# Performance work log

Measured on AMD Instinct MI355X. Metric: run time of the kernel, lower is better.

The kernel has to match this reference:

```python
import jax, jax.numpy as jnp
import numpy as np

D_MODEL = 2048
N_HEADS = 16
KV_HEADS = 4
HEAD_DIM = D_MODEL // N_HEADS            # 128
GROUP = N_HEADS // KV_HEADS              # 4
KV_WIDTH = KV_HEADS * HEAD_DIM           # 512
B, T = 2, 2048


def setup_inputs() -> dict:
    key = jax.random.key(0)
    ks = jax.random.split(key, 5)
    s = 0.02
    x = jax.random.normal(ks[0], (B, T, D_MODEL), dtype=jnp.float32)
    attn_mask = jnp.tril(jnp.ones((T, T), dtype=bool))  # causal
    qkv_w = jax.random.normal(ks[1], (D_MODEL, D_MODEL + 2 * KV_WIDTH), dtype=jnp.float32) * s
    qkv_b = jax.random.normal(ks[2], (D_MODEL + 2 * KV_WIDTH,), dtype=jnp.float32) * s
    proj_w = jax.random.normal(ks[3], (D_MODEL, D_MODEL), dtype=jnp.float32) * s
    proj_b = jax.random.normal(ks[4], (D_MODEL,), dtype=jnp.float32) * s
    return {"x": x, "attn_mask": attn_mask, "qkv_w": qkv_w, "qkv_b": qkv_b,
            "proj_w": proj_w, "proj_b": proj_b}


def reference(x, attn_mask, qkv_w, qkv_b, proj_w, proj_b):
    b, t, c = x.shape
    qkv = x @ qkv_w + qkv_b                               # [b,t,3072]
    q = qkv[..., :D_MODEL]
    k = qkv[..., D_MODEL:D_MODEL + KV_WIDTH]
    v = qkv[..., D_MODEL + KV_WIDTH:]
    # q: [b, kv_heads, group, t, d]; k,v: [b, kv_heads, t, d]
    q = q.reshape(b, t, KV_HEADS, GROUP, HEAD_DIM).transpose(0, 2, 3, 1, 4)
    k = k.reshape(b, t, KV_HEADS, HEAD_DIM).transpose(0, 2, 1, 3)
    v = v.reshape(b, t, KV_HEADS, HEAD_DIM).transpose(0, 2, 1, 3)
    scale = 1.0 / jnp.sqrt(jnp.asarray(HEAD_DIM, dtype=x.dtype))
    att = jnp.einsum('bkgtd,bksd->bkgts', q, k) * scale   # [b,kv,g,t,t]
    att = jnp.where(attn_mask, att, jnp.asarray(-jnp.inf, dtype=att.dtype))
    att = jax.nn.softmax(att, axis=-1)
    out = jnp.einsum('bkgts,bksd->bkgtd', att, v)         # [b,kv,g,t,d]
    out = out.transpose(0, 3, 1, 2, 4).reshape(b, t, c)
    return out @ proj_w + proj_b
```

## Files before the change

### kernel.cpp

```cpp
#include <hip/hip_runtime.h>
#include <cstdint>
#include <cstddef>

#define D_MODEL 2048
#define T_SEQ   2048
#define BATCH   2
#define N_HEADS 16
#define KV_HEADS 4
#define HEAD_DIM 128
#define QKV_N   3072
#define ROWS    (BATCH * T_SEQ)

typedef float  floatx4 __attribute__((ext_vector_type(4)));
typedef short  shortx8 __attribute__((ext_vector_type(8)));
typedef __bf16 bf16x8  __attribute__((ext_vector_type(8)));

typedef const void __attribute__((address_space(1))) gvoid_t;
typedef void __attribute__((address_space(3)))       svoid_t;

__device__ __forceinline__ floatx4 mfma16(shortx8 a, shortx8 b, floatx4 c) {
  return __builtin_amdgcn_mfma_f32_16x16x32_bf16(
      __builtin_bit_cast(bf16x8, a), __builtin_bit_cast(bf16x8, b), c, 0, 0, 0);
}

__device__ __forceinline__ unsigned short f2bf(float f) {
  union { float f; unsigned int u; } v; v.f = f;
  unsigned int u = v.u;
  u += 0x7fffu + ((u >> 16) & 1u);
  return (unsigned short)(u >> 16);
}

__device__ __forceinline__ unsigned short f2bf_hw(float f) {
  return __builtin_bit_cast(unsigned short, (__bf16)f);
}

__global__ void cvt_x(const float* __restrict__ in, unsigned short* __restrict__ out, int n4) {
  int i = blockIdx.x * blockDim.x + threadIdx.x;
  if (i >= n4) return;
  float4 v = ((const float4*)in)[i];
  ushort4 o;
  o.x = f2bf(v.x); o.y = f2bf(v.y); o.z = f2bf(v.z); o.w = f2bf(v.w);
  ((ushort4*)out)[i] = o;
}

__global__ void transpose_cvt(const float* __restrict__ W, unsigned short* __restrict__ Wt,
                              int K, int N) {
  __shared__ float tile[32][33];
  int n0 = blockIdx.x * 32, k0 = blockIdx.y * 32;
  int tx = threadIdx.x, ty = threadIdx.y;
  #pragma unroll
  for (int i = 0; i < 32; i += 8)
    tile[ty + i][tx] = W[(size_t)(k0 + ty + i) * N + n0 + tx];
  __syncthreads();
  #pragma unroll
  for (int i = 0; i < 32; i += 8)
    Wt[(size_t)(n0 + ty + i) * K + k0 + tx] = f2bf(tile[tx][ty + i]);
}

__global__ void build_kt(const unsigned short* __restrict__ qkv, unsigned short* __restrict__ kst) {
  int o = blockIdx.x * blockDim.x + threadIdx.x;
  int t   = o & 2047;
  int d8  = (o >> 11) & 15;
  int kvh = (o >> 15) & 3;
  int b   = o >> 17;
  uint4 v = *(const uint4*)(qkv + (size_t)(b * T_SEQ + t) * QKV_N
                            + D_MODEL + kvh * HEAD_DIM + d8 * 8);
  *(uint4*)(kst + (size_t)o * 8) = v;
}

__global__ void build_vt(const unsigned short* __restrict__ qkv, unsigned short* __restrict__ vst) {
  int o = blockIdx.x * blockDim.x + threadIdx.x;
  int d   = o & 127;
  int t8  = (o >> 7) & 255;
  int kvh = (o >> 15) & 3;
  int b   = o >> 17;
  const unsigned short* src = qkv + (size_t)(b * T_SEQ + t8 * 8) * QKV_N
                              + D_MODEL + 512 + kvh * HEAD_DIM + d;
  union { unsigned short s[8]; uint4 v; } tmp;
  #pragma unroll
  for (int j = 0; j < 8; ++j) tmp.s[j] = src[(size_t)j * QKV_N];
  *(uint4*)(vst + (size_t)o * 8) = tmp.v;
}

__global__ __launch_bounds__(512, 2) void gemm256(
    const unsigned short* __restrict__ A,
    const unsigned short* __restrict__ Bt,
    const float* __restrict__ bias,
    void* __restrict__ Cout,
    int M, int N, int K, int c_bf16)
{
  __shared__ __align__(16) unsigned short lds[65536];
  const int tid  = threadIdx.x;
  const int wave = tid >> 6, lane = tid & 63;
  const int quad = lane >> 4, l16 = lane & 15;
  const int wr = wave >> 2, wc = wave & 3;
  const int bm = blockIdx.y * 256, bn = blockIdx.x * 256;
  const int NT = K >> 6;

  const int r0 = tid >> 3;
  const int cx = (tid & 7) ^ (r0 & 7);
  const size_t K64 = (size_t)64 * K;
  const unsigned short* a_src = A  + (size_t)(bm + r0) * K + cx * 8;
  const unsigned short* b_src = Bt + (size_t)(bn + r0) * K + cx * 8;
  const int wOff = wave * 512;

  #define LDSA_(buf, half) (lds + (((buf) << 1) + (half)) * 8192)
  #define LDSB_(buf, half) (lds + 32768 + (((buf) << 1) + (half)) * 8192)
  #define KOFF(h, t) ((size_t)(h) * 128 * K + (size_t)(t) * 64)
  #define STAGE(srcbase, ldshalf, koff) do {                                          \
    __builtin_amdgcn_global_load_lds((gvoid_t*)((srcbase) + (koff)),                  \
        (svoid_t*)((ldshalf) + wOff), 16, 0, 0);                                      \
    __builtin_amdgcn_global_load_lds((gvoid_t*)((srcbase) + (koff) + K64),            \
        (svoid_t*)((ldshalf) + wOff + 4096), 16, 0, 0);                               \
  } while (0)

  const int rowA = (wr * 64 + l16) * 64;
  const int rowB = (wc * 32 + l16) * 64;
  const int xo0 = ((quad)     ^ (l16 & 7)) * 8;
  const int xo1 = ((4 + quad) ^ (l16 & 7)) * 8;

  floatx4 acc[8][4] = {};
  shortx8 Afr[4][2];
  shortx8 Bfr[4][2];

  STAGE(a_src, LDSA_(0, 0), KOFF(0, 0));
  STAGE(b_src, LDSB_(0, 0), KOFF(0, 0));
  STAGE(b_src, LDSB_(0, 1), KOFF(1, 0));
  STAGE(a_src, LDSA_(0, 1), KOFF(1, 0));
  if (NT > 1) {
    STAGE(a_src, LDSA_(1, 0), KOFF(0, 1));
    STAGE(b_src, LDSB_(1, 0), KOFF(0, 1));
    STAGE(b_src, LDSB_(1, 1), KOFF(1, 1));
  }

  for (int t = 0; t < NT; ++t) {
    const int buf = t & 1;
    unsigned short* sA0 = LDSA_(buf, 0);
    unsigned short* sA1 = LDSA_(buf, 1);
    unsigned short* sB0 = LDSB_(buf, 0);
    unsigned short* sB1 = LDSB_(buf, 1);

    if (t == NT - 1) asm volatile("s_waitcnt vmcnt(0)" ::: "memory");
    else             asm volatile("s_waitcnt vmcnt(6)" ::: "memory");
    __builtin_amdgcn_s_barrier();
    #pragma unroll
    for (int mi = 0; mi < 4; ++mi) {
      Afr[mi][0] = *(const shortx8*)(sA0 + rowA + mi * 1024 + xo0);
      Afr[mi][1] = *(const shortx8*)(sA0 + rowA + mi * 1024 + xo1);
    }
    #pragma unroll
    for (int ni = 0; ni < 2; ++ni) {
      Bfr[ni][0] = *(const shortx8*)(sB0 + rowB + ni * 1024 + xo0);
      Bfr[ni][1] = *(const shortx8*)(sB0 + rowB + ni * 1024 + xo1);
    }
    if (t + 1 < NT) STAGE(a_src, LDSA_(buf ^ 1, 1), KOFF(1, t + 1));
    asm volatile("s_waitcnt lgkmcnt(0)" ::: "memory");
    __builtin_amdgcn_s_setprio(1);
    #pragma unroll
    for (int ks = 0; ks < 2; ++ks)
      #pragma unroll
      for (int mi = 0; mi < 4; ++mi)
        #pragma unroll
        for (int ni = 0; ni < 2; ++ni)
          acc[mi][ni] = mfma16(Afr[mi][ks], Bfr[ni][ks], acc[mi][ni]);
    __builtin_amdgcn_s_setprio(0);
    __builtin_amdgcn_s_barrier();

    #pragma unroll
    for (int ni = 0; ni < 2; ++ni) {
      Bfr[2 + ni][0] = *(const shortx8*)(sB1 + rowB + ni * 1024 + xo0);
      Bfr[2 + ni][1] = *(const shortx8*)(sB1 + rowB + ni * 1024 + xo1);
    }
    if (t + 2 < NT) STAGE(a_src, LDSA_(buf, 0), KOFF(0, t + 2));
    __builtin_amdgcn_s_barrier();
    asm volatile("s_waitcnt lgkmcnt(0)" ::: "memory");
    __builtin_amdgcn_s_setprio(1);
    #pragma unroll
    for (int ks = 0; ks < 2; ++ks)
      #pragma unroll
      for (int mi = 0; mi < 4; ++mi)
        #pragma unroll
        for (int ni = 0; ni < 2; ++ni)
          acc[mi][2 + ni] = mfma16(Afr[mi][ks], Bfr[2 + ni][ks], acc[mi][2 + ni]);
    __builtin_amdgcn_s_setprio(0);
    __builtin_amdgcn_s_barrier();

    #pragma unroll
    for (int mi = 0; mi < 4; ++mi) {
      Afr[mi][0] = *(const shortx8*)(sA1 + rowA + mi * 1024 + xo0);
      Afr[mi][1] = *(const shortx8*)(sA1 + rowA + mi * 1024 + xo1);
    }
    if (t + 2 < NT) STAGE(b_src, LDSB_(buf, 0), KOFF(0, t + 2));
    __builtin_amdgcn_s_barrier();
    asm volatile("s_waitcnt lgkmcnt(0)" ::: "memory");
    __builtin_amdgcn_s_setprio(1);
    #pragma unroll
    for (int ks = 0; ks < 2; ++ks)
      #pragma unroll
      for (int mi = 0; mi < 4; ++mi)
        #pragma unroll
        for (int ni = 0; ni < 2; ++ni)
          acc[4 + mi][2 + ni] = mfma16(Afr[mi][ks], Bfr[2 + ni][ks], acc[4 + mi][2 + ni]);
    __builtin_amdgcn_s_setprio(0);
    __builtin_amdgcn_s_barrier();

    if (t + 2 < NT) STAGE(b_src, LDSB_(buf, 1), KOFF(1, t + 2));
    __builtin_amdgcn_s_barrier();
    __builtin_amdgcn_s_setprio(1);
    #pragma unroll
    for (int ks = 0; ks < 2; ++ks)
      #pragma unroll
      for (int mi = 0; mi < 4; ++mi)
        #pragma unroll
        for (int ni = 0; ni < 2; ++ni)
          acc[4 + mi][ni] = mfma16(Afr[mi][ks], Bfr[ni][ks], acc[4 + mi][ni]);
    __builtin_amdgcn_s_setprio(0);
    __builtin_amdgcn_s_barrier();
  }

  #pragma unroll
  for (int mi = 0; mi < 8; ++mi) {
    const int row = bm + (mi >> 2) * 128 + wr * 64 + (mi & 3) * 16 + quad * 4;
    #pragma unroll
    for (int ni = 0; ni < 4; ++ni) {
      const int col = bn + (ni >> 1) * 128 + wc * 32 + (ni & 1) * 16 + l16;
      const float bv = bias[col];
      #pragma unroll
      for (int r = 0; r < 4; ++r) {
        float v = acc[mi][ni][r] + bv;
        if (c_bf16)
          ((unsigned short*)Cout)[(size_t)(row + r) * N + col] = f2bf_hw(v);
        else
          ((float*)Cout)[(size_t)(row + r) * N + col] = v;
      }
    }
  }
  #undef LDSA_
  #undef LDSB_
  #undef KOFF
  #undef STAGE
}

__global__ __launch_bounds__(256) void attn_kernel(
    const unsigned short* __restrict__ qkv,
    const unsigned short* __restrict__ kst,
    const unsigned short* __restrict__ vst,
    unsigned short* __restrict__ aout)
{
  __shared__ __align__(16) unsigned short sK[2][16 * 64 * 8];
  __shared__ __align__(16) unsigned short sV[2][8 * 128 * 8];
  __shared__ __align__(16) unsigned short sP[4][8 * 16 * 8];

  const int tid  = threadIdx.x;
  const int wave = tid >> 6, lane = tid & 63;
  const int quad = lane >> 4, l16 = lane & 15;
  const int head = blockIdx.y, b = blockIdx.z;
  const int kvh = head >> 2;
  const float cf = 0.08838834764831845f * 1.4426950408889634f;
  const float THR = 25.0f;

  const unsigned short* kbase = kst + (size_t)((b * KV_HEADS + kvh) * 16) * 2048 * 8;
  const unsigned short* vbase = vst + (size_t)((b * KV_HEADS + kvh) * 256) * 128 * 8;
  unsigned short* sPw = sP[wave];

  #define STAGE_KV(dst, kb_) do {                                              \
    _Pragma("unroll")                                                          \
    for (int it_ = 0; it_ < 4; ++it_) {                                        \
      const int c_ = it_ * 4 + wave;                                           \
      __builtin_amdgcn_global_load_lds(                                        \
          (gvoid_t*)(kbase + ((size_t)c_ * 2048 + (kb_)) * 8 + lane * 8),      \
          (svoid_t*)(&sK[dst][c_ * 512]), 16, 0, 0);                           \
    }                                                                          \
    const unsigned short* vt_ = vbase + (size_t)((kb_) >> 3) * 128 * 8;        \
    _Pragma("unroll")                                                          \
    for (int it_ = 0; it_ < 4; ++it_) {                                        \
      const int c_ = it_ * 4 + wave;                                           \
      __builtin_amdgcn_global_load_lds(                                        \
          (gvoid_t*)(vt_ + c_ * 512 + lane * 8),                               \
          (svoid_t*)(&sV[dst][c_ * 512]), 16, 0, 0);                           \
    }                                                                          \
  } while (0)

  #pragma unroll 1
  for (int half = 0; half < 2; ++half) {
    const int qt = half ? blockIdx.x : (31 - blockIdx.x);
    const int q0 = qt * 64;

    shortx8 qf[4];
    {
      const unsigned short* qp = qkv + (size_t)(b * T_SEQ + q0 + wave * 16 + l16) * QKV_N
                                 + head * HEAD_DIM + quad * 8;
      #pragma unroll
      for (int ks = 0; ks < 4; ++ks)
        qf[ks] = *(const shortx8*)(qp + ks * 32);
    }

    float m_i[4], l_i[4];
    #pragma unroll
    for (int r = 0; r < 4; ++r) { m_i[r] = -__builtin_inff(); l_i[r] = 0.f; }
    floatx4 o_acc[8] = {};

    STAGE_KV(0, 0);

    for (int kt = 0; kt <= qt; ++kt) {
      const int cur = kt & 1;
      const unsigned short* sKc = sK[cur];
      const unsigned short* sVc = sV[cur];

      if (kt < qt) {
        STAGE_KV(cur ^ 1, (kt + 1) * 64);
        asm volatile("s_waitcnt vmcnt(8)" ::: "memory");
      } else {
        asm volatile("s_waitcnt vmcnt(0)" ::: "memory");
      }
      __builtin_amdgcn_s_barrier();

      floatx4 s[4] = {};
      __builtin_amdgcn_s_setprio(1);
      #pragma unroll
      for (int ks = 0; ks < 4; ++ks) {
        #pragma unroll
        for (int ct = 0; ct < 4; ++ct) {
          shortx8 kf = *(const shortx8*)&sKc[((ks * 4 + quad) * 64 + ct * 16 + l16) * 8];
          s[ct] = mfma16(qf[ks], kf, s[ct]);
        }
      }
      __builtin_amdgcn_s_setprio(0);

      if (kt == qt) {
        const int qrow = q0 + wave * 16 + quad * 4;
        const int kb = kt * 64;
        #pragma unroll
        for (int ct = 0; ct < 4; ++ct) {
          const int kcol = kb + ct * 16 + l16;
          #pragma unroll
          for (int r = 0; r < 4; ++r)
            if (kcol > qrow + r) s[ct][r] = -__builtin_inff();
        }
      }

      float mx[4];
      #pragma unroll
      for (int r = 0; r < 4; ++r) {
        float m = fmaxf(fmaxf(s[0][r], s[1][r]), fmaxf(s[2][r], s[3][r]));
        m = fmaxf(m, __shfl_xor(m, 1));
        m = fmaxf(m, __shfl_xor(m, 2));
        m = fmaxf(m, __shfl_xor(m, 4));
        m = fmaxf(m, __shfl_xor(m, 8));
        mx[r] = m;
      }

      if (__ballot((mx[0] > m_i[0] + THR) || (mx[1] > m_i[1] + THR) ||
                   (mx[2] > m_i[2] + THR) || (mx[3] > m_i[3] + THR))) {
        float alpha_r[4];
        #pragma unroll
        for (int r = 0; r < 4; ++r) {
          const float newm = fmaxf(m_i[r], mx[r]);
          alpha_r[r] = exp2f((m_i[r] - newm) * cf);
          m_i[r] = newm;
          l_i[r] *= alpha_r[r];
        }
        #pragma unroll
        for (int nt = 0; nt < 8; ++nt)
          #pragma unroll
          for (int r = 0; r < 4; ++r) o_acc[nt][r] *= alpha_r[r];
      }

      #pragma unroll
      for (int r = 0; r < 4; ++r) {
        const float nmc = m_i[r] * cf;
        float p0 = exp2f(fmaf(s[0][r], cf, -nmc));
        float p1 = exp2f(fmaf(s[1][r], cf, -nmc));
        float p2 = exp2f(fmaf(s[2][r], cf, -nmc));
        float p3 = exp2f(fmaf(s[3][r], cf, -nmc));
        s[0][r] = p0; s[1][r] = p1; s[2][r] = p2; s[3][r] = p3;
        l_i[r] += (p0 + p1) + (p2 + p3);
      }

      #pragma unroll
      for (int ct = 0; ct < 4; ++ct)
        #pragma unroll
        for (int r = 0; r < 4; ++r)
          sPw[((ct * 2 + (l16 >> 3)) * 16 + quad * 4 + r) * 8 + (l16 & 7)] = f2bf_hw(s[ct][r]);
      __asm__ __volatile__("s_waitcnt lgkmcnt(0)" ::: "memory");

      __builtin_amdgcn_s_setprio(1);
      #pragma unroll
      for (int ks = 0; ks < 2; ++ks) {
        shortx8 pf = *(const shortx8*)&sPw[((ks * 4 + quad) * 16 + l16) * 8];
        #pragma unroll
        for (int nt = 0; nt < 8; ++nt) {
          shortx8 vf = *(const shortx8*)&sVc[((ks * 4 + quad) * 128 + nt * 16 + l16) * 8];
          o_acc[nt] = mfma16(pf, vf, o_acc[nt]);
        }
      }
      __builtin_amdgcn_s_setprio(0);

      asm volatile("s_waitcnt lgkmcnt(0)" ::: "memory");
      __builtin_amdgcn_s_barrier();
    }

    const int trow = q0 + wave * 16 + quad * 4;
    #pragma unroll
    for (int r = 0; r < 4; ++r) {
      float l = l_i[r];
      l += __shfl_xor(l, 1);
      l += __shfl_xor(l, 2);
      l += __shfl_xor(l, 4);
      l += __shfl_xor(l, 8);
      const float inv = 1.f / l;
      #pragma unroll
      for (int nt = 0; nt < 8; ++nt) {
        aout[(size_t)(b * T_SEQ + trow + r) * D_MODEL + head * HEAD_DIM + nt * 16 + l16] =
            f2bf_hw(o_acc[nt][r] * inv);
      }
    }
  }
  #undef STAGE_KV
}

extern "C" void kernel_launch(void* const* d_in, const int* in_sizes, int n_in,
                              void* d_out, int out_size, void* d_ws, size_t ws_size,
                              hipStream_t stream) {
  const float* x      = (const float*)d_in[0];
  const float* qkv_w  = (const float*)d_in[2];
  const float* qkv_b  = (const float*)d_in[3];
  const float* proj_w = (const float*)d_in[4];
  const float* proj_b = (const float*)d_in[5];
  float* out = (float*)d_out;

  char* ws = (char*)d_ws;
  unsigned short* x_bf    = (unsigned short*)(ws);
  unsigned short* qkvw_t  = (unsigned short*)(ws + (size_t)16777216);
  unsigned short* projw_t = (unsigned short*)(ws + (size_t)29360128);
  unsigned short* qkvbuf  = (unsigned short*)(ws + (size_t)37748736);
  unsigned short* vstaged = (unsigned short*)(ws + (size_t)62914560);
  unsigned short* kstaged = qkvw_t;
  unsigned short* attn_out = x_bf;

  cvt_x<<<(ROWS * D_MODEL / 4 + 255) / 256, 256, 0, stream>>>(x, x_bf, ROWS * D_MODEL / 4);
  transpose_cvt<<<dim3(QKV_N / 32, D_MODEL / 32), dim3(32, 8), 0, stream>>>(qkv_w, qkvw_t, D_MODEL, QKV_N);
  transpose_cvt<<<dim3(D_MODEL / 32, D_MODEL / 32), dim3(32, 8), 0, stream>>>(proj_w, projw_t, D_MODEL, D_MODEL);
  gemm256<<<dim3(QKV_N / 256, ROWS / 256), 512, 0, stream>>>(
      x_bf, qkvw_t, qkv_b, (void*)qkvbuf, ROWS, QKV_N, D_MODEL, 1);
  build_kt<<<1024, 256, 0, stream>>>(qkvbuf, kstaged);
  build_vt<<<1024, 256, 0, stream>>>(qkvbuf, vstaged);
  attn_kernel<<<dim3(16, N_HEADS, BATCH), 256, 0, stream>>>(qkvbuf, kstaged, vstaged, attn_out);
  gemm256<<<dim3(D_MODEL / 256, ROWS / 256), 512, 0, stream>>>(
      attn_out, projw_t, proj_b, (void*)out, ROWS, D_MODEL, D_MODEL, 0);
}
```

Measured before the change: 341.1 us.

## Split attention KV loop across two wave groups with LDS merge

The attention block grows from 4 to 8 waves. Two groups of four waves process even and odd KV tiles for the same 64 query rows, and their online-softmax partial results (m, l, O) are merged through LDS at the end. The goal is more parallelism per block on the sequential causal KV loop, halving its length per wave. In exchange, the double-buffered prefetch pipeline is replaced by a synchronous load-then-wait every iteration. It also adds barriers, a merge step, and higher register pressure under launch_bounds(512,4).

Result: faster. 329.6 us (-3.4%).

```diff
diff --git a/kernel.cpp b/kernel.cpp
--- a/kernel.cpp
+++ b/kernel.cpp
@@ -241,7 +241,7 @@
   #undef STAGE
 }
 
-__global__ __launch_bounds__(256) void attn_kernel(
+__global__ __launch_bounds__(512, 4) void attn_kernel(
     const unsigned short* __restrict__ qkv,
     const unsigned short* __restrict__ kst,
     const unsigned short* __restrict__ vst,
@@ -249,10 +249,11 @@
 {
   __shared__ __align__(16) unsigned short sK[2][16 * 64 * 8];
   __shared__ __align__(16) unsigned short sV[2][8 * 128 * 8];
-  __shared__ __align__(16) unsigned short sP[4][8 * 16 * 8];
+  __shared__ __align__(16) unsigned short sP[8][4 * 16 * 8];
 
   const int tid  = threadIdx.x;
   const int wave = tid >> 6, lane = tid & 63;
+  const int split = wave >> 2, g = wave & 3;
   const int quad = lane >> 4, l16 = lane & 15;
   const int head = blockIdx.y, b = blockIdx.z;
   const int kvh = head >> 2;
@@ -263,21 +264,24 @@
   const unsigned short* vbase = vst + (size_t)((b * KV_HEADS + kvh) * 256) * 128 * 8;
   unsigned short* sPw = sP[wave];
 
-  #define STAGE_KV(dst, kb_) do {                                              \
+  float* mrgO  = (float*)&sK[0][0];
+  float* mrgML = (float*)&sV[0][0];
+
+  #define STAGE_KV(sp, kb_) do {                                               \
     _Pragma("unroll")                                                          \
     for (int it_ = 0; it_ < 4; ++it_) {                                        \
-      const int c_ = it_ * 4 + wave;                                           \
+      const int c_ = it_ * 4 + g;                                              \
       __builtin_amdgcn_global_load_lds(                                        \
           (gvoid_t*)(kbase + ((size_t)c_ * 2048 + (kb_)) * 8 + lane * 8),      \
-          (svoid_t*)(&sK[dst][c_ * 512]), 16, 0, 0);                           \
+          (svoid_t*)(&sK[sp][c_ * 512]), 16, 0, 0);                            \
     }                                                                          \
     const unsigned short* vt_ = vbase + (size_t)((kb_) >> 3) * 128 * 8;        \
     _Pragma("unroll")                                                          \
     for (int it_ = 0; it_ < 4; ++it_) {                                        \
-      const int c_ = it_ * 4 + wave;                                           \
+      const int c_ = it_ * 4 + g;                                              \
       __builtin_amdgcn_global_load_lds(                                        \
           (gvoid_t*)(vt_ + c_ * 512 + lane * 8),                               \
-          (svoid_t*)(&sV[dst][c_ * 512]), 16, 0, 0);                           \
+          (svoid_t*)(&sV[sp][c_ * 512]), 16, 0, 0);                            \
     }                                                                          \
   } while (0)
 
@@ -288,7 +292,7 @@
 
     shortx8 qf[4];
     {
-      const unsigned short* qp = qkv + (size_t)(b * T_SEQ + q0 + wave * 16 + l16) * QKV_N
+      const unsigned short* qp = qkv + (size_t)(b * T_SEQ + q0 + g * 16 + l16) * QKV_N
                                  + head * HEAD_DIM + quad * 8;
       #pragma unroll
       for (int ks = 0; ks < 4; ++ks)
@@ -300,119 +304,150 @@
     for (int r = 0; r < 4; ++r) { m_i[r] = -__builtin_inff(); l_i[r] = 0.f; }
     floatx4 o_acc[8] = {};
 
-    STAGE_KV(0, 0);
-
-    for (int kt = 0; kt <= qt; ++kt) {
-      const int cur = kt & 1;
-      const unsigned short* sKc = sK[cur];
-      const unsigned short* sVc = sV[cur];
-
-      if (kt < qt) {
-        STAGE_KV(cur ^ 1, (kt + 1) * 64);
-        asm volatile("s_waitcnt vmcnt(8)" ::: "memory");
-      } else {
-        asm volatile("s_waitcnt vmcnt(0)" ::: "memory");
+    const int J = (qt >> 1) + 1;
+    for (int j = 0; j < J; ++j) {
+      const int kt = 2 * j + split;
+      const bool act = (kt <= qt);
+
+      __builtin_amdgcn_s_barrier();
+      if (act) STAGE_KV(split, kt * 64);
+      asm volatile("s_waitcnt vmcnt(0)" ::: "memory");
+      __builtin_amdgcn_s_barrier();
+
+      if (act) {
+        floatx4 s[4] = {};
+        __builtin_amdgcn_s_setprio(1);
+        #pragma unroll
+        for (int ks = 0; ks < 4; ++ks) {
+          #pragma unroll
+          for (int ct = 0; ct < 4; ++ct) {
+            shortx8 kf = *(const shortx8*)&sK[split][((ks * 4 + quad) * 64 + ct * 16 + l16) * 8];
+            s[ct] = mfma16(qf[ks], kf, s[ct]);
+          }
+        }
+        __builtin_amdgcn_s_setprio(0);
+
+        if (kt == qt) {
+          const int qrow = q0 + g * 16 + quad * 4;
+          const int kb = kt * 64;
+          #pragma unroll
+          for (int ct = 0; ct < 4; ++ct) {
+            const int kcol = kb + ct * 16 + l16;
+            #pragma unroll
+            for (int r = 0; r < 4; ++r)
+              if (kcol > qrow + r) s[ct][r] = -__builtin_inff();
+          }
+        }
+
+        float mx[4];
+        #pragma unroll
+        for (int r = 0; r < 4; ++r) {
+          float m = fmaxf(fmaxf(s[0][r], s[1][r]), fmaxf(s[2][r], s[3][r]));
+          m = fmaxf(m, __shfl_xor(m, 1));
+          m = fmaxf(m, __shfl_xor(m, 2));
+          m = fmaxf(m, __shfl_xor(m, 4));
+          m = fmaxf(m, __shfl_xor(m, 8));
+          mx[r] = m;
+        }
+
+        if (__ballot((mx[0] > m_i[0] + THR) || (mx[1] > m_i[1] + THR) ||
+                     (mx[2] > m_i[2] + THR) || (mx[3] > m_i[3] + THR))) {
+          float alpha_r[4];
+          #pragma unroll
+          for (int r = 0; r < 4; ++r) {
+            const float newm = fmaxf(m_i[r], mx[r]);
+            alpha_r[r] = exp2f((m_i[r] - newm) * cf);
+            m_i[r] = newm;
+            l_i[r] *= alpha_r[r];
+          }
+          #pragma unroll
+          for (int nt = 0; nt < 8; ++nt)
+            #pragma unroll
+            for (int r = 0; r < 4; ++r) o_acc[nt][r] *= alpha_r[r];
+        }
+
+        #pragma unroll
+        for (int r = 0; r < 4; ++r) {
+          const float nmc = m_i[r] * cf;
+          float p0 = exp2f(fmaf(s[0][r], cf, -nmc));
+          float p1 = exp2f(fmaf(s[1][r], cf, -nmc));
+          float p2 = exp2f(fmaf(s[2][r], cf, -nmc));
+          float p3 = exp2f(fmaf(s[3][r], cf, -nmc));
+          s[0][r] = p0; s[1][r] = p1; s[2][r] = p2; s[3][r] = p3;
+          l_i[r] += (p0 + p1) + (p2 + p3);
+        }
+
+        #pragma unroll
+        for (int c = 0; c < 2; ++c) {
+          #pragma unroll
+          for (int ctl = 0; ctl < 2; ++ctl) {
+            const int ct = c * 2 + ctl;
+            #pragma unroll
+            for (int r = 0; r < 4; ++r)
+              sPw[((ctl * 2 + (l16 >> 3)) * 16 + quad * 4 + r) * 8 + (l16 & 7)] =
+                  f2bf_hw(s[ct][r]);
+          }
+          __asm__ __volatile__("s_waitcnt lgkmcnt(0)" ::: "memory");
+          shortx8 pf = *(const shortx8*)&sPw[(quad * 16 + l16) * 8];
+          __builtin_amdgcn_s_setprio(1);
+          #pragma unroll
+          for (int nt = 0; nt < 8; ++nt) {
+            shortx8 vf = *(const shortx8*)&sV[split][((c * 4 + quad) * 128 + nt * 16 + l16) * 8];
+            o_acc[nt] = mfma16(pf, vf, o_acc[nt]);
+          }
+          __builtin_amdgcn_s_setprio(0);
+        }
       }
-      __builtin_amdgcn_s_barrier();
-
-      floatx4 s[4] = {};
-      __builtin_amdgcn_s_setprio(1);
-      #pragma unroll
-      for (int ks = 0; ks < 4; ++ks) {
-        #pragma unroll
-        for (int ct = 0; ct < 4; ++ct) {
-          shortx8 kf = *(const shortx8*)&sKc[((ks * 4 + quad) * 64 + ct * 16 + l16) * 8];
-          s[ct] = mfma16(qf[ks], kf, s[ct]);
-        }
+    }
+
+    __builtin_amdgcn_s_barrier();
+    if (split == 1) {
+      #pragma unroll
+      for (int nt = 0; nt < 8; ++nt)
+        #pragma unroll
+        for (int r = 0; r < 4; ++r)
+          mrgO[g * 2048 + (quad * 4 + r) * 128 + nt * 16 + l16] = o_acc[nt][r];
+      #pragma unroll
+      for (int r = 0; r < 4; ++r) {
+        mrgML[(g * 64 + lane) * 8 + r * 2]     = m_i[r];
+        mrgML[(g * 64 + lane) * 8 + r * 2 + 1] = l_i[r];
       }
-      __builtin_amdgcn_s_setprio(0);
-
-      if (kt == qt) {
-        const int qrow = q0 + wave * 16 + quad * 4;
-        const int kb = kt * 64;
-        #pragma unroll
-        for (int ct = 0; ct < 4; ++ct) {
-          const int kcol = kb + ct * 16 + l16;
-          #pragma unroll
-          for (int r = 0; r < 4; ++r)
-            if (kcol > qrow + r) s[ct][r] = -__builtin_inff();
-        }
+    }
+    asm volatile("s_waitcnt lgkmcnt(0)" ::: "memory");
+    __builtin_amdgcn_s_barrier();
+
+    if (split == 0) {
+      float lm[4], a0[4], a1[4];
+      #pragma unroll
+      for (int r = 0; r < 4; ++r) {
+        const float m1 = mrgML[(g * 64 + lane) * 8 + r * 2];
+        const float l1 = mrgML[(g * 64 + lane) * 8 + r * 2 + 1];
+        const float M = fmaxf(m_i[r], m1);
+        a0[r] = exp2f((m_i[r] - M) * cf);
+        a1[r] = exp2f((m1 - M) * cf);
+        lm[r] = a0[r] * l_i[r] + a1[r] * l1;
       }
-
-      float mx[4];
+      #pragma unroll
+      for (int nt = 0; nt < 8; ++nt)
+        #pragma unroll
+        for (int r = 0; r < 4; ++r)
+          o_acc[nt][r] = a0[r] * o_acc[nt][r]
+                       + a1[r] * mrgO[g * 2048 + (quad * 4 + r) * 128 + nt * 16 + l16];
+
+      const int trow = q0 + g * 16 + quad * 4;
       #pragma unroll
       for (int r = 0; r < 4; ++r) {
-        float m = fmaxf(fmaxf(s[0][r], s[1][r]), fmaxf(s[2][r], s[3][r]));
-        m = fmaxf(m, __shfl_xor(m, 1));
-        m = fmaxf(m, __shfl_xor(m, 2));
-        m = fmaxf(m, __shfl_xor(m, 4));
-        m = fmaxf(m, __shfl_xor(m, 8));
-        mx[r] = m;
-      }
-
-      if (__ballot((mx[0] > m_i[0] + THR) || (mx[1] > m_i[1] + THR) ||
-                   (mx[2] > m_i[2] + THR) || (mx[3] > m_i[3] + THR))) {
-        float alpha_r[4];
-        #pragma unroll
-        for (int r = 0; r < 4; ++r) {
-          const float newm = fmaxf(m_i[r], mx[r]);
-          alpha_r[r] = exp2f((m_i[r] - newm) * cf);
-          m_i[r] = newm;
-          l_i[r] *= alpha_r[r];
-        }
-        #pragma unroll
-        for (int nt = 0; nt < 8; ++nt)
-          #pragma unroll
-          for (int r = 0; r < 4; ++r) o_acc[nt][r] *= alpha_r[r];
-      }
-
-      #pragma unroll
-      for (int r = 0; r < 4; ++r) {
-        const float nmc = m_i[r] * cf;
-        float p0 = exp2f(fmaf(s[0][r], cf, -nmc));
-        float p1 = exp2f(fmaf(s[1][r], cf, -nmc));
-        float p2 = exp2f(fmaf(s[2][r], cf, -nmc));
-        float p3 = exp2f(fmaf(s[3][r], cf, -nmc));
-        s[0][r] = p0; s[1][r] = p1; s[2][r] = p2; s[3][r] = p3;
-        l_i[r] += (p0 + p1) + (p2 + p3);
-      }
-
-      #pragma unroll
-      for (int ct = 0; ct < 4; ++ct)
-        #pragma unroll
-        for (int r = 0; r < 4; ++r)
-          sPw[((ct * 2 + (l16 >> 3)) * 16 + quad * 4 + r) * 8 + (l16 & 7)] = f2bf_hw(s[ct][r]);
-      __asm__ __volatile__("s_waitcnt lgkmcnt(0)" ::: "memory");
-
-      __builtin_amdgcn_s_setprio(1);
-      #pragma unroll
-      for (int ks = 0; ks < 2; ++ks) {
-        shortx8 pf = *(const shortx8*)&sPw[((ks * 4 + quad) * 16 + l16) * 8];
+        float l = lm[r];
+        l += __shfl_xor(l, 1);
+        l += __shfl_xor(l, 2);
+        l += __shfl_xor(l, 4);
+        l += __shfl_xor(l, 8);
+        const float inv = 1.f / l;
         #pragma unroll
         for (int nt = 0; nt < 8; ++nt) {
-          shortx8 vf = *(const shortx8*)&sVc[((ks * 4 + quad) * 128 + nt * 16 + l16) * 8];
-          o_acc[nt] = mfma16(pf, vf, o_acc[nt]);
-        }
-      }
-      __builtin_amdgcn_s_setprio(0);
-
-      asm volatile("s_waitcnt lgkmcnt(0)" ::: "memory");
-      __builtin_amdgcn_s_barrier();
-    }
-
-    const int trow = q0 + wave * 16 + quad * 4;
-    #pragma unroll
-    for (int r = 0; r < 4; ++r) {
-      float l = l_i[r];
-      l += __shfl_xor(l, 1);
-      l += __shfl_xor(l, 2);
-      l += __shfl_xor(l, 4);
-      l += __shfl_xor(l, 8);
-      const float inv = 1.f / l;
-      #pragma unroll
-      for (int nt = 0; nt < 8; ++nt) {
-        aout[(size_t)(b * T_SEQ + trow + r) * D_MODEL + head * HEAD_DIM + nt * 16 + l16] =
-            f2bf_hw(o_acc[nt][r] * inv);
+          aout[(size_t)(b * T_SEQ + trow + r) * D_MODEL + head * HEAD_DIM + nt * 16 + l16] =
+              f2bf_hw(o_acc[nt][r] * inv);
+        }
       }
     }
   }
@@ -445,7 +480,7 @@
       x_bf, qkvw_t, qkv_b, (void*)qkvbuf, ROWS, QKV_N, D_MODEL, 1);
   build_kt<<<1024, 256, 0, stream>>>(qkvbuf, kstaged);
   build_vt<<<1024, 256, 0, stream>>>(qkvbuf, vstaged);
-  attn_kernel<<<dim3(16, N_HEADS, BATCH), 256, 0, stream>>>(qkvbuf, kstaged, vstaged, attn_out);
+  attn_kernel<<<dim3(16, N_HEADS, BATCH), 512, 0, stream>>>(qkvbuf, kstaged, vstaged, attn_out);
   gemm256<<<dim3(D_MODEL / 256, ROWS / 256), 512, 0, stream>>>(
       attn_out, projw_t, proj_b, (void*)out, ROWS, D_MODEL, D_MODEL, 0);
 }
```
